# Kernel tuning notes

Measured on AMD Instinct MI355X. Metric: run time of the kernel, lower is better.

## Reference

```python
import jax, jax.numpy as jnp
import numpy as np

B, S, V, E, H, NL, DFF = 16, 16, 64, 64, 8, 4, 2048
L = S * V
DH = E // H
NUM_GRIDS = 100
POI_DIM = 8
OV_DIM = 8


def setup_inputs() -> dict:
    key = jax.random.key(0)
    ks = jax.random.split(key, 32)
    sc = 0.05
    inp = {}
    inp['features'] = jax.random.normal(ks[0], (B, S, V, 3), jnp.float32)
    inp['overlap_tag'] = jax.random.randint(ks[1], (B, S, V), 0, 3)
    inp['poi_id'] = jax.random.randint(ks[2], (B, S, V), 0, NUM_GRIDS + 1)
    # embedders
    inp['W_raw'] = jax.random.normal(ks[3], (3, E), jnp.float32) * sc
    inp['b_raw'] = jnp.zeros((E,), jnp.float32)
    inp['pos_tab'] = jax.random.normal(ks[4], (S, E), jnp.float32) * sc
    inp['type_tab'] = jax.random.normal(ks[5], (V, E), jnp.float32) * sc
    inp['poi_tab'] = jax.random.normal(ks[6], (NUM_GRIDS + 1, POI_DIM), jnp.float32) * sc
    inp['overlap_tab'] = jax.random.normal(ks[7], (3, OV_DIM), jnp.float32) * sc
    inp['W_comb'] = jax.random.normal(ks[8], (E + OV_DIM + POI_DIM, E), jnp.float32) * sc
    inp['b_comb'] = jnp.zeros((E,), jnp.float32)
    # transformer layers (stacked over NL)
    inp['Wqkv'] = jax.random.normal(ks[9], (NL, E, 3 * E), jnp.float32) * sc
    inp['bqkv'] = jnp.zeros((NL, 3 * E), jnp.float32)
    inp['Wo'] = jax.random.normal(ks[10], (NL, E, E), jnp.float32) * sc
    inp['bo'] = jnp.zeros((NL, E), jnp.float32)
    inp['ln1_s'] = jnp.ones((NL, E), jnp.float32)
    inp['ln1_b'] = jnp.zeros((NL, E), jnp.float32)
    inp['W1'] = jax.random.normal(ks[11], (NL, E, DFF), jnp.float32) * sc
    inp['b1'] = jnp.zeros((NL, DFF), jnp.float32)
    inp['W2'] = jax.random.normal(ks[12], (NL, DFF, E), jnp.float32) * sc
    inp['b2'] = jnp.zeros((NL, E), jnp.float32)
    inp['ln2_s'] = jnp.ones((NL, E), jnp.float32)
    inp['ln2_b'] = jnp.zeros((NL, E), jnp.float32)
    inp['W_head'] = jax.random.normal(ks[13], (E, 3), jnp.float32) * sc
    inp['b_head'] = jnp.zeros((3,), jnp.float32)
    return inp


def _layer_norm(x, s, b):
    m = x.mean(-1, keepdims=True)
    v = ((x - m) ** 2).mean(-1, keepdims=True)
    return (x - m) / jnp.sqrt(v + 1e-5) * s + b


def _forward(features, overlap_tag, poi_id, W_raw, b_raw, pos_tab, type_tab,
             poi_tab, overlap_tab, W_comb, b_comb, Wqkv, bqkv, Wo, bo,
             ln1_s, ln1_b, W1, b1, W2, b2, ln2_s, ln2_b, W_head, b_head):
    # padding_idx=0 rows are zero (as in nn.Embedding(padding_idx=0))
    poi_tab = poi_tab.at[0].set(0.0)
    overlap_tab = overlap_tab.at[0].set(0.0)

    zero_mask = (features.sum(-1) == 0).reshape(B, L)  # [B, L]
    ov_idx = jnp.maximum(overlap_tag, 0)
    poi_idx = jnp.maximum(poi_id, 0)

    feat_e = features @ W_raw + b_raw                    # [B,S,V,E]
    concat = jnp.concatenate([feat_e, overlap_tab[ov_idx], poi_tab[poi_idx]], axis=-1)
    x = (concat @ W_comb + b_comb).reshape(B, L, E)      # [B,L,E]

    t_idx = jnp.repeat(jnp.arange(S), V)                 # [L]
    v_idx = jnp.tile(jnp.arange(V), S)                   # [L]
    struct_mask = (t_idx[:, None] != t_idx[None, :]) & (v_idx[:, None] != v_idx[None, :])
    full_mask = struct_mask[None] | zero_mask[:, None, :] | zero_mask[:, :, None]  # [B,L,L]
    bias = jnp.where(full_mask, -jnp.inf, 0.0)[:, None, :, :]  # [B,1,L,L]

    x = x + pos_tab[t_idx][None] + type_tab[v_idx][None]

    scale = 1.0 / jnp.sqrt(jnp.asarray(DH, x.dtype))
    for l in range(NL):
        qkv = x @ Wqkv[l] + bqkv[l]                      # [B,L,3E]
        q, k, v = jnp.split(qkv, 3, axis=-1)
        q = q.reshape(B, L, H, DH)
        k = k.reshape(B, L, H, DH)
        v = v.reshape(B, L, H, DH)
        scores = jnp.einsum('bqhd,bkhd->bhqk', q, k) * scale + bias
        attn = jax.nn.softmax(scores, axis=-1)
        o = jnp.einsum('bhqk,bkhd->bqhd', attn, v).reshape(B, L, E)
        x = _layer_norm(x + o @ Wo[l] + bo[l], ln1_s[l], ln1_b[l])
        ff = jax.nn.relu(x @ W1[l] + b1[l]) @ W2[l] + b2[l]
        x = _layer_norm(x + ff, ln2_s[l], ln2_b[l])

    last = x.reshape(B, S, V, E)[:, -1]                  # [B,V,E]
    return last @ W_head + b_head                        # [B,V,3]


def reference(features, overlap_tag, poi_id, W_raw, b_raw, pos_tab, type_tab,
              poi_tab, overlap_tab, W_comb, b_comb, Wqkv, bqkv, Wo, bo,
              ln1_s, ln1_b, W1, b1, W2, b2, ln2_s, ln2_b, W_head, b_head):
    return _forward(features, overlap_tag, poi_id, W_raw, b_raw, pos_tab, type_tab,
                    poi_tab, overlap_tab, W_comb, b_comb, Wqkv, bqkv, Wo, bo,
                    ln1_s, ln1_b, W1, b1, W2, b2, ln2_s, ln2_b, W_head, b_head)
```

## Files before the change

### kernel.cpp

```cpp
#include <hip/hip_runtime.h>
#include <math.h>

#define BB 16
#define SS 16
#define VVV 64
#define EE 64
#define HHH 8
#define NLAYER 4
#define DFF_ 2048
#define LL 1024
#define BL 16384
#define PERL 131072

typedef __attribute__((ext_vector_type(8))) _Float16 half8;
typedef __attribute__((ext_vector_type(4))) _Float16 half4v;
typedef __attribute__((ext_vector_type(2))) _Float16 half2v;
typedef __attribute__((ext_vector_type(4))) float f32x4;

#if defined(__has_builtin)
#if __has_builtin(__builtin_amdgcn_fdot2)
#define HAVE_FDOT2 1
#endif
#endif

#define SW64(m, k)  (((m) << 6) + ((((k) >> 3) ^ ((m) & 7)) << 3) + ((k) & 7))


__global__ __launch_bounds__(256) void k_prep(
    const float* __restrict__ W1, const float* __restrict__ W2,
    const float* __restrict__ Wqkv, const float* __restrict__ Wo,
    const float* __restrict__ Wcomb,
    _Float16* __restrict__ w1f, _Float16* __restrict__ w2f,
    _Float16* __restrict__ wqkvf, _Float16* __restrict__ wof,
    _Float16* __restrict__ wcombt)
{
  __shared__ float t[64 * 65];
  int bx = blockIdx.x;
  int cc = threadIdx.x & 63, rr = threadIdx.x >> 6;

  if (bx >= 272) {
    int r0 = (bx - 272) * 64;
#pragma unroll
    for (int i = 0; i < 16; i++) {
      int r = i * 4 + rr;
      if (r0 + r < 80) t[r * 65 + cc] = Wcomb[(size_t)(r0 + r) * 64 + cc];
    }
    __syncthreads();
#pragma unroll
    for (int i = 0; i < 16; i++) {
      int c = i * 4 + rr;
      if (r0 + c < 80) wcombt[(size_t)cc * 80 + r0 + c] = (_Float16)t[c * 65 + cc];
    }
    return;
  }

  const float* src; _Float16* dst; int astr;
  if (bx < 128) {
    int l = bx >> 5, g = bx & 31;
    src = W1 + (size_t)l * PERL + g * 64; astr = 2048;
    dst = w1f + (size_t)(l * 32 + g) * 4096;
  } else if (bx < 256) {
    int j = bx - 128; int l = j >> 5, g = j & 31;
    src = W2 + (size_t)l * PERL + (size_t)g * 64 * 64; astr = 64;
    dst = w2f + (size_t)(l * 32 + g) * 4096;
  } else if (bx < 268) {
    int j = bx - 256; int l = j / 3, g = j % 3;
    src = Wqkv + (size_t)l * 64 * 192 + g * 64; astr = 192;
    dst = wqkvf + (size_t)(l * 3 + g) * 4096;
  } else {
    int l = bx - 268;
    src = Wo + (size_t)l * 4096; astr = 64;
    dst = wof + (size_t)l * 4096;
  }
#pragma unroll
  for (int i = 0; i < 16; i++) {
    int a = i * 4 + rr;
    t[cc * 65 + a] = src[(size_t)a * astr + cc];
  }
  __syncthreads();
#pragma unroll
  for (int it = 0; it < 2; it++) {
    int c = threadIdx.x + it * 256;
    int frag = c >> 6, lane = c & 63;
    int m = (frag >> 1) * 16 + (lane & 15);
    int k0 = (frag & 1) * 32 + (lane >> 4) * 8;
    const float* tr = &t[m * 65 + k0];
    half8 h;
#pragma unroll
    for (int j = 0; j < 8; j++) h[j] = (_Float16)tr[j];
    *(half8*)&dst[(size_t)c * 8] = h;
  }
}

__device__ __forceinline__ void qkv_nb(
    const half8 (&af)[2][2], const _Float16* __restrict__ wqkvf,
    const float* __restrict__ bqkv, _Float16* __restrict__ qbuf,
    _Float16* __restrict__ kbuf, _Float16* __restrict__ vbuf,
    int bx, int nb, int wm, int wn, int lane)
{
  int quad = lane >> 4, l15 = lane & 15;
  const _Float16* bt = wqkvf + (size_t)nb * 4096;
  half8 bf[2][2];
#pragma unroll
  for (int nt = 0; nt < 2; nt++)
#pragma unroll
    for (int ks = 0; ks < 2; ks++)
      bf[nt][ks] = *(const half8*)&bt[(size_t)(((wn * 2 + nt) * 2 + ks) * 512) +
                                      lane * 8];
  f32x4 acc[2][2];
#pragma unroll
  for (int mt = 0; mt < 2; mt++)
#pragma unroll
    for (int nt = 0; nt < 2; nt++) {
      float bv = bqkv[nb * 64 + wn * 32 + nt * 16 + l15];
      acc[mt][nt] = (f32x4){bv, bv, bv, bv};
    }
#pragma unroll
  for (int ks = 0; ks < 2; ks++)
#pragma unroll
    for (int mt = 0; mt < 2; mt++)
#pragma unroll
      for (int nt = 0; nt < 2; nt++)
        acc[mt][nt] = __builtin_amdgcn_mfma_f32_16x16x32_f16(
            af[mt][ks], bf[nt][ks], acc[mt][nt], 0, 0, 0);
  _Float16* dst = (nb == 0) ? qbuf : ((nb == 1) ? kbuf : vbuf);
#pragma unroll
  for (int mt = 0; mt < 2; mt++)
#pragma unroll
    for (int nt = 0; nt < 2; nt++) {
      int col = wn * 32 + nt * 16 + l15;
      int h = col >> 3, d = col & 7;
#pragma unroll
      for (int r = 0; r < 4; r++) {
        int row = bx * 64 + wm * 32 + mt * 16 + quad * 4 + r;
        int b = row >> 10, rb = row & 1023;
        dst[((size_t)(b * 8 + h) * 1024 + rb) * 8 + d] = (_Float16)acc[mt][nt][r];
      }
    }
}

__device__ __forceinline__ void ffn_load(
    const _Float16* __restrict__ w1f, const _Float16* __restrict__ w2f, int g,
    half8 (&a1)[2][2], half8 (&b2w)[2][2], int wm, int wn, int lane)
{
  const _Float16* w1t_ = w1f + (size_t)g * 4096;
  const _Float16* w2t_ = w2f + (size_t)g * 4096;
#pragma unroll
  for (int ht = 0; ht < 2; ht++)
#pragma unroll
    for (int ks = 0; ks < 2; ks++)
      a1[ht][ks] = *(const half8*)&w1t_[(size_t)(((wm * 2 + ht) * 2 + ks) * 512) +
                                        lane * 8];
#pragma unroll
  for (int nt = 0; nt < 2; nt++)
#pragma unroll
    for (int ks = 0; ks < 2; ks++)
      b2w[nt][ks] = *(const half8*)&w2t_[(size_t)(((wn * 2 + nt) * 2 + ks) * 512) +
                                         lane * 8];
}

__device__ __forceinline__ void ffn_step(
    const half8 (&a1)[2][2], const half8 (&b2w)[2][2], const half8 (&xb)[2][2],
    _Float16* hsbuf, const float* __restrict__ b1, int g, f32x4 (&acc)[2][2],
    int wm, int wn, int lane)
{
  int quad = lane >> 4, l15 = lane & 15;
  f32x4 hacc[2][2];
#pragma unroll
  for (int ht = 0; ht < 2; ht++)
#pragma unroll
    for (int mt = 0; mt < 2; mt++) hacc[ht][mt] = (f32x4){0.f, 0.f, 0.f, 0.f};
#pragma unroll
  for (int ks = 0; ks < 2; ks++)
#pragma unroll
    for (int ht = 0; ht < 2; ht++)
#pragma unroll
      for (int mt = 0; mt < 2; mt++)
        hacc[ht][mt] = __builtin_amdgcn_mfma_f32_16x16x32_f16(
            a1[ht][ks], xb[mt][ks], hacc[ht][mt], 0, 0, 0);
#pragma unroll
  for (int ht = 0; ht < 2; ht++) {
    float4 bb = *(const float4*)&b1[g * 64 + wm * 32 + ht * 16 + quad * 4];
#pragma unroll
    for (int mt = 0; mt < 2; mt++) {
      f32x4 hv = hacc[ht][mt];
      half4v hp = (half4v){
          (_Float16)fmaxf(hv[0] + bb.x, 0.f), (_Float16)fmaxf(hv[1] + bb.y, 0.f),
          (_Float16)fmaxf(hv[2] + bb.z, 0.f), (_Float16)fmaxf(hv[3] + bb.w, 0.f)};
      *(half4v*)&hsbuf[SW64(wn * 32 + mt * 16 + l15,
                            wm * 32 + ht * 16 + quad * 4)] = hp;
    }
  }
  __syncthreads();
#pragma unroll
  for (int ks = 0; ks < 2; ks++)
#pragma unroll
    for (int mt = 0; mt < 2; mt++) {
      half8 a2 = *(const half8*)&hsbuf[SW64(wm * 32 + mt * 16 + l15,
                                            ks * 32 + quad * 8)];
#pragma unroll
      for (int nt = 0; nt < 2; nt++)
        acc[mt][nt] = __builtin_amdgcn_mfma_f32_16x16x32_f16(a2, b2w[nt][ks],
                                                             acc[mt][nt], 0, 0, 0);
    }
}

__global__ __launch_bounds__(256) void k_embqkv(
    const float* __restrict__ features, const int* __restrict__ ovtag,
    const int* __restrict__ poiid, const float* __restrict__ W_raw,
    const float* __restrict__ b_raw, const float* __restrict__ ov_tab,
    const float* __restrict__ poi_tab, const _Float16* __restrict__ wcombt,
    const float* __restrict__ b_comb, const float* __restrict__ pos_tab,
    const float* __restrict__ type_tab, float* __restrict__ x1,
    float* __restrict__ zm, const _Float16* __restrict__ wqkvf,
    const float* __restrict__ bqkv, _Float16* __restrict__ qbuf,
    _Float16* __restrict__ kbuf, _Float16* __restrict__ vbuf)
{
  constexpr int KP = 104;
  __shared__ _Float16 As[64 * KP];
  __shared__ _Float16 Bs[64 * KP];
  __shared__ _Float16 xs[4096];
  int tid = threadIdx.x;
  int bx = blockIdx.x;
  int m0 = bx * 64;
  int wave = tid >> 6, lane = tid & 63, quad = lane >> 4, l15 = lane & 15;
  int wm = wave >> 1, wn = wave & 1;
  for (int p = tid; p < 1536; p += 256) {
    int r = p / 24, s = p - r * 24; int c = s * 4;
    int row = m0 + r;
    float f0 = features[row * 3 + 0];
    float f1 = features[row * 3 + 1];
    float f2 = features[row * 3 + 2];
    if (s == 0) zm[row] = ((f0 + f1 + f2) == 0.f) ? 1.f : 0.f;
    half4v h;
#pragma unroll
    for (int j = 0; j < 4; j++) {
      int cc = c + j; float v;
      if (cc < 64) {
        v = b_raw[cc] + f0 * W_raw[cc] + f1 * W_raw[64 + cc] + f2 * W_raw[128 + cc];
      } else if (cc < 72) {
        int tt = ovtag[row]; v = (tt <= 0) ? 0.f : ov_tab[tt * 8 + cc - 64];
      } else if (cc < 80) {
        int tt = poiid[row]; v = (tt <= 0) ? 0.f : poi_tab[tt * 8 + cc - 72];
      } else v = 0.f;
      h[j] = (_Float16)v;
    }
    *(half4v*)&As[r * KP + c] = h;
  }
  for (int p = tid; p < 1536; p += 256) {
    int r = p / 24, s = p - r * 24; int c = s * 4;
    half4v h = (half4v){0, 0, 0, 0};
    if (c < 80) h = *(const half4v*)&wcombt[r * 80 + c];
    *(half4v*)&Bs[r * KP + c] = h;
  }
  __syncthreads();
  f32x4 acc[2][2];
#pragma unroll
  for (int mt = 0; mt < 2; mt++)
#pragma unroll
    for (int nt = 0; nt < 2; nt++) {
      float bv = b_comb[wn * 32 + nt * 16 + l15];
      acc[mt][nt] = (f32x4){bv, bv, bv, bv};
    }
#pragma unroll
  for (int ks = 0; ks < 3; ks++) {
    half8 af[2], bf[2];
#pragma unroll
    for (int mt = 0; mt < 2; mt++)
      af[mt] = *(const half8*)&As[(wm * 32 + mt * 16 + l15) * KP + ks * 32 + quad * 8];
#pragma unroll
    for (int nt = 0; nt < 2; nt++)
      bf[nt] = *(const half8*)&Bs[(wn * 32 + nt * 16 + l15) * KP + ks * 32 + quad * 8];
#pragma unroll
    for (int mt = 0; mt < 2; mt++)
#pragma unroll
      for (int nt = 0; nt < 2; nt++)
        acc[mt][nt] = __builtin_amdgcn_mfma_f32_16x16x32_f16(af[mt], bf[nt],
                                                             acc[mt][nt], 0, 0, 0);
  }
#pragma unroll
  for (int mt = 0; mt < 2; mt++)
#pragma unroll
    for (int nt = 0; nt < 2; nt++)
#pragma unroll
      for (int r = 0; r < 4; r++) {
        int lrow = wm * 32 + mt * 16 + quad * 4 + r;
        int row = m0 + lrow;
        int col = wn * 32 + nt * 16 + l15;
        int l = row & (LL - 1);
        float v = acc[mt][nt][r] +
            pos_tab[(l >> 6) * 64 + col] + type_tab[(l & 63) * 64 + col];
        x1[(size_t)row * 64 + col] = v;
        xs[SW64(lrow, col)] = (_Float16)v;
      }
  __syncthreads();
  half8 af[2][2];
#pragma unroll
  for (int mt = 0; mt < 2; mt++)
#pragma unroll
    for (int ks = 0; ks < 2; ks++)
      af[mt][ks] = *(const half8*)&xs[SW64(wm * 32 + mt * 16 + l15,
                                           ks * 32 + quad * 8)];
  for (int nb = 0; nb < 3; nb++)
    qkv_nb(af, wqkvf, bqkv, qbuf, kbuf, vbuf, bx, nb, wm, wn, lane);
}

__global__ __launch_bounds__(256) void k_attn2(
    const _Float16* __restrict__ qbuf, const _Float16* __restrict__ kbuf,
    const _Float16* __restrict__ vbuf, const float* __restrict__ zm,
    _Float16* __restrict__ obuf)
{
  __shared__ _Float16 Ks[1024 * 8];
  __shared__ _Float16 Vs[1024 * 8];
  __shared__ float zs[1024];
  int blk = blockIdx.x;
  int qb = blk & 3, h = (blk >> 2) & 7, b = blk >> 5;
  int qrow = qb * 256 + threadIdx.x;
  half8 qh = *(const half8*)&qbuf[(size_t)(b * 8 + h) * 8192 + (size_t)qrow * 8];
  const _Float16* kb = kbuf + (size_t)(b * 8 + h) * 8192;
  const _Float16* vb = vbuf + (size_t)(b * 8 + h) * 8192;
  for (int p = threadIdx.x; p < 1024; p += 256) {
    *(half8*)&Ks[p * 8] = *(const half8*)&kb[p * 8];
    *(half8*)&Vs[p * 8] = *(const half8*)&vb[p * 8];
    zs[p] = zm[b * LL + p];
  }
  __syncthreads();
  int tq = qrow >> 6, vq = qrow & 63;
  const float scale = 0.3535533905932738f;
  float m = -INFINITY, lsum = 0.f;
  float acc[8] = {0.f, 0.f, 0.f, 0.f, 0.f, 0.f, 0.f, 0.f};
  bool zmq = (zs[qrow] != 0.f);

  auto attend = [&](int k) {
    if (zs[k] != 0.f) return;
    half8 kk = *(const half8*)&Ks[k * 8];
    float s = 0.f;
#ifdef HAVE_FDOT2
#pragma unroll
    for (int j = 0; j < 4; j++) {
      half2v qa = (half2v){qh[2 * j], qh[2 * j + 1]};
      half2v ka = (half2v){kk[2 * j], kk[2 * j + 1]};
      s = __builtin_amdgcn_fdot2(qa, ka, s, false);
    }
#else
#pragma unroll
    for (int j = 0; j < 8; j++) s += (float)qh[j] * (float)kk[j];
#endif
    s *= scale;
    half8 vv = *(const half8*)&Vs[k * 8];
    if (s <= m) {
      float p = __expf(s - m);
      lsum += p;
#pragma unroll
      for (int d = 0; d < 8; d++) acc[d] += p * (float)vv[d];
    } else {
      float r = __expf(m - s);
      lsum = lsum * r + 1.f;
#pragma unroll
      for (int d = 0; d < 8; d++) acc[d] = acc[d] * r + (float)vv[d];
      m = s;
    }
  };

  if (!zmq) {
    for (int vv = 0; vv < 64; vv++) attend(tq * 64 + vv);
    for (int tt = 0; tt < 16; tt++) {
      if (tt == tq) continue;
      attend(tt * 64 + vq);
    }
  }
  float inv = 1.f / lsum;
  half8 o;
#pragma unroll
  for (int d = 0; d < 8; d++) o[d] = (_Float16)(acc[d] * inv);
  size_t tile = (size_t)(b * 16 + (qrow >> 6));
  int frag = ((qrow >> 4) & 3) * 2 + (h >> 2);
  int flane = (h & 3) * 16 + (qrow & 15);
  *(half8*)&obuf[tile * 4096 + frag * 512 + flane * 8] = o;
}

__global__ __launch_bounds__(512) void k_layer(
    const _Float16* __restrict__ obuf, const _Float16* __restrict__ wof,
    const float* __restrict__ bo, float* __restrict__ x1,
    const float* __restrict__ ln1_s, const float* __restrict__ ln1_b,
    const _Float16* __restrict__ w1f, const _Float16* __restrict__ w2f,
    const float* __restrict__ b1, const float* __restrict__ b2,
    const float* __restrict__ ln2_s, const float* __restrict__ ln2_b,
    const _Float16* __restrict__ wqkvf, const float* __restrict__ bqkv,
    _Float16* __restrict__ qbuf, _Float16* __restrict__ kbuf,
    _Float16* __restrict__ vbuf, int doqkv,
    const float* __restrict__ Wh, const float* __restrict__ bh,
    float* __restrict__ out)
{
  __shared__ float ots[64 * 68];
  __shared__ _Float16 xs[4096];
  __shared__ float x2f[4096];
  __shared__ _Float16 hs[2][2][4096];
  int tid = threadIdx.x;
  int bx = blockIdx.x;
  int wave = tid >> 6, lane = tid & 63;
  int quad = lane >> 4, l15 = lane & 15;
  int grp = wave >> 2, w4 = wave & 3;
  int wm = w4 >> 1, wn = w4 & 1;

  {
    const _Float16* ot = obuf + (size_t)bx * 4096;
    int mq = grp * 2 + wm;
    half8 af[2], bf[2][2];
#pragma unroll
    for (int ks = 0; ks < 2; ks++)
      af[ks] = *(const half8*)&ot[(size_t)((mq * 2 + ks) * 512) + lane * 8];
#pragma unroll
    for (int nt = 0; nt < 2; nt++)
#pragma unroll
      for (int ks = 0; ks < 2; ks++)
        bf[nt][ks] = *(const half8*)&wof[(size_t)(((wn * 2 + nt) * 2 + ks) * 512) +
                                         lane * 8];
    f32x4 acc[2];
#pragma unroll
    for (int nt = 0; nt < 2; nt++) {
      float bv = bo[wn * 32 + nt * 16 + l15];
      acc[nt] = (f32x4){bv, bv, bv, bv};
    }
#pragma unroll
    for (int ks = 0; ks < 2; ks++)
#pragma unroll
      for (int nt = 0; nt < 2; nt++)
        acc[nt] = __builtin_amdgcn_mfma_f32_16x16x32_f16(af[ks], bf[nt][ks],
                                                         acc[nt], 0, 0, 0);
#pragma unroll
    for (int nt = 0; nt < 2; nt++)
#pragma unroll
      for (int r = 0; r < 4; r++)
        ots[(mq * 16 + quad * 4 + r) * 68 + wn * 32 + nt * 16 + l15] = acc[nt][r];
  }
  __syncthreads();
  for (int i = 0; i < 8; i++) {
    int row = wave * 8 + i;
    size_t off = (size_t)(bx * 64 + row) * 64 + lane;
    float val = ots[row * 68 + lane] + x1[off];
    float sum = val;
#pragma unroll
    for (int o = 32; o > 0; o >>= 1) sum += __shfl_xor(sum, o);
    float mean = sum * (1.f / 64.f);
    float d = val - mean;
    float sq = d * d;
#pragma unroll
    for (int o = 32; o > 0; o >>= 1) sq += __shfl_xor(sq, o);
    float xv = d * rsqrtf(sq * (1.f / 64.f) + 1e-5f) * ln1_s[lane] + ln1_b[lane];
    x2f[row * 64 + lane] = xv;
    xs[SW64(row, lane)] = (_Float16)xv;
  }
  __syncthreads();

  half8 xb[2][2];
#pragma unroll
  for (int mt = 0; mt < 2; mt++)
#pragma unroll
    for (int ks = 0; ks < 2; ks++)
      xb[mt][ks] = *(const half8*)&xs[SW64(wn * 32 + mt * 16 + l15,
                                           ks * 32 + quad * 8)];
  f32x4 acc[2][2];
#pragma unroll
  for (int mt = 0; mt < 2; mt++)
#pragma unroll
    for (int nt = 0; nt < 2; nt++) {
      float bv = (grp == 0) ? b2[wn * 32 + nt * 16 + l15] : 0.f;
      acc[mt][nt] = (f32x4){bv, bv, bv, bv};
    }
  half8 a1x[2][2], b2x[2][2], a1y[2][2], b2y[2][2];
  ffn_load(w1f, w2f, grp, a1x, b2x, wm, wn, lane);
  for (int ii = 0; ii < 8; ii++) {
    ffn_load(w1f, w2f, ii * 4 + 2 + grp, a1y, b2y, wm, wn, lane);
    ffn_step(a1x, b2x, xb, &hs[grp][0][0], b1, ii * 4 + grp, acc, wm, wn, lane);
    if (ii < 7) ffn_load(w1f, w2f, ii * 4 + 4 + grp, a1x, b2x, wm, wn, lane);
    ffn_step(a1y, b2y, xb, &hs[grp][1][0], b1, ii * 4 + 2 + grp, acc, wm, wn, lane);
  }
  __syncthreads();
  if (grp == 0) {
#pragma unroll
    for (int mt = 0; mt < 2; mt++)
#pragma unroll
      for (int nt = 0; nt < 2; nt++)
#pragma unroll
        for (int r = 0; r < 4; r++)
          ots[(wm * 32 + mt * 16 + quad * 4 + r) * 68 + wn * 32 + nt * 16 + l15] =
              acc[mt][nt][r];
  }
  __syncthreads();
  if (grp == 1) {
#pragma unroll
    for (int mt = 0; mt < 2; mt++)
#pragma unroll
      for (int nt = 0; nt < 2; nt++)
#pragma unroll
        for (int r = 0; r < 4; r++)
          ots[(wm * 32 + mt * 16 + quad * 4 + r) * 68 + wn * 32 + nt * 16 + l15] +=
              acc[mt][nt][r];
  }
  __syncthreads();
  for (int i = 0; i < 8; i++) {
    int row = wave * 8 + i;
    size_t off = (size_t)(bx * 64 + row) * 64 + lane;
    float val = ots[row * 68 + lane] + x2f[row * 64 + lane];
    float sum = val;
#pragma unroll
    for (int o = 32; o > 0; o >>= 1) sum += __shfl_xor(sum, o);
    float mean = sum * (1.f / 64.f);
    float d = val - mean;
    float sq = d * d;
#pragma unroll
    for (int o = 32; o > 0; o >>= 1) sq += __shfl_xor(sq, o);
    float xv = d * rsqrtf(sq * (1.f / 64.f) + 1e-5f) * ln2_s[lane] + ln2_b[lane];
    x1[off] = xv;
    x2f[row * 64 + lane] = xv;
    xs[SW64(row, lane)] = (_Float16)xv;
  }
  if (!doqkv) {
    __syncthreads();
    if ((bx & 15) == 15 && tid < 192) {
      int b = bx >> 4;
      int v = tid / 3, j = tid - v * 3;
      float a = bh[j];
      for (int e = 0; e < 64; e++)
        a += x2f[v * 64 + e] * Wh[e * 3 + j];
      out[((size_t)(b * 64 + v)) * 3 + j] = a;
    }
    return;
  }
  __syncthreads();
  half8 af[2][2];
#pragma unroll
  for (int mt = 0; mt < 2; mt++)
#pragma unroll
    for (int ks = 0; ks < 2; ks++)
      af[mt][ks] = *(const half8*)&xs[SW64(wm * 32 + mt * 16 + l15,
                                           ks * 32 + quad * 8)];
  for (int nb = grp; nb < 3; nb += 2)
    qkv_nb(af, wqkvf, bqkv, qbuf, kbuf, vbuf, bx, nb, wm, wn, lane);
}

extern "C" void kernel_launch(void* const* d_in, const int* in_sizes, int n_in,
                              void* d_out, int out_size, void* d_ws, size_t ws_size,
                              hipStream_t stream) {
  const float* features = (const float*)d_in[0];
  const int*   ovtag    = (const int*)d_in[1];
  const int*   poiid    = (const int*)d_in[2];
  const float* W_raw    = (const float*)d_in[3];
  const float* b_raw    = (const float*)d_in[4];
  const float* pos_tab  = (const float*)d_in[5];
  const float* type_tab = (const float*)d_in[6];
  const float* poi_tab  = (const float*)d_in[7];
  const float* ov_tab   = (const float*)d_in[8];
  const float* W_comb   = (const float*)d_in[9];
  const float* b_comb   = (const float*)d_in[10];
  const float* Wqkv     = (const float*)d_in[11];
  const float* bqkv     = (const float*)d_in[12];
  const float* Wo       = (const float*)d_in[13];
  const float* bo       = (const float*)d_in[14];
  const float* ln1_s    = (const float*)d_in[15];
  const float* ln1_b    = (const float*)d_in[16];
  const float* W1       = (const float*)d_in[17];
  const float* b1       = (const float*)d_in[18];
  const float* W2       = (const float*)d_in[19];
  const float* b2       = (const float*)d_in[20];
  const float* ln2_s    = (const float*)d_in[21];
  const float* ln2_b    = (const float*)d_in[22];
  const float* W_head   = (const float*)d_in[23];
  const float* b_head   = (const float*)d_in[24];
  float* out = (float*)d_out;
  float* ws  = (float*)d_ws;

  float* zm  = ws;
  float* x1  = zm + BL;
  _Float16* qbuf   = (_Float16*)(x1 + (size_t)BL * 64);
  _Float16* kbuf   = qbuf + (size_t)BL * 64;
  _Float16* vbuf   = kbuf + (size_t)BL * 64;
  _Float16* obuf16 = vbuf + (size_t)BL * 64;
  _Float16* wcombt = obuf16 + (size_t)BL * 64;
  _Float16* w1f    = wcombt + 5120;
  _Float16* w2f    = w1f + (size_t)NLAYER * PERL;
  _Float16* wqkvf  = w2f + (size_t)NLAYER * PERL;
  _Float16* wof    = wqkvf + (size_t)NLAYER * 3 * 4096;

  k_prep<<<274, 256, 0, stream>>>(W1, W2, Wqkv, Wo, W_comb,
                                  w1f, w2f, wqkvf, wof, wcombt);
  k_embqkv<<<256, 256, 0, stream>>>(features, ovtag, poiid, W_raw, b_raw,
                                    ov_tab, poi_tab, wcombt, b_comb,
                                    pos_tab, type_tab, x1, zm,
                                    wqkvf, bqkv, qbuf, kbuf, vbuf);
  for (int l = 0; l < NLAYER; l++) {
    k_attn2<<<512, 256, 0, stream>>>(qbuf, kbuf, vbuf, zm, obuf16);
    int doqkv = (l < NLAYER - 1);
    k_layer<<<256, 512, 0, stream>>>(
        obuf16, wof + (size_t)l * 4096, bo + l * EE, x1,
        ln1_s + l * EE, ln1_b + l * EE,
        w1f + (size_t)l * PERL, w2f + (size_t)l * PERL,
        b1 + l * DFF_, b2 + l * EE,
        ln2_s + l * EE, ln2_b + l * EE,
        wqkvf + (size_t)(l + 1 < NLAYER ? l + 1 : 0) * 3 * 4096,
        bqkv + (l + 1 < NLAYER ? l + 1 : 0) * 192,
        qbuf, kbuf, vbuf, doqkv, W_head, b_head, out);
  }
}
```

Measured before the change: 317.4 us.

## Halve per-block row tiles in layer and attention kernels to double grid size

The fused layer kernel now handles 32 rows per block with 256 threads instead of 64 rows with 512, and asks for two blocks per CU. Its FFN, output projection and QKV projection are re-indexed to match, with the QKV projection inlined per wave. The attention kernel uses 128-thread blocks over 1024 blocks, and its online softmax update becomes a branchless max/rescale form. The aim is more blocks for better CU occupancy and less divergence, at the cost of loading each K/V head twice as often and reading FFN weights once per 32 rows rather than per 64.

Result: faster. 309.0 us (-2.7%).

```diff
diff --git a/kernel.cpp b/kernel.cpp
--- a/kernel.cpp
+++ b/kernel.cpp
@@ -139,9 +139,9 @@
     }
 }
 
-__device__ __forceinline__ void ffn_load(
+__device__ __forceinline__ void ffn_load2(
     const _Float16* __restrict__ w1f, const _Float16* __restrict__ w2f, int g,
-    half8 (&a1)[2][2], half8 (&b2w)[2][2], int wm, int wn, int lane)
+    half8 (&a1)[2][2], half8 (&b2w)[2][2], int wn, int lane)
 {
   const _Float16* w1t_ = w1f + (size_t)g * 4096;
   const _Float16* w2t_ = w2f + (size_t)g * 4096;
@@ -149,7 +149,7 @@
   for (int ht = 0; ht < 2; ht++)
 #pragma unroll
     for (int ks = 0; ks < 2; ks++)
-      a1[ht][ks] = *(const half8*)&w1t_[(size_t)(((wm * 2 + ht) * 2 + ks) * 512) +
+      a1[ht][ks] = *(const half8*)&w1t_[(size_t)(((wn * 2 + ht) * 2 + ks) * 512) +
                                         lane * 8];
 #pragma unroll
   for (int nt = 0; nt < 2; nt++)
@@ -159,10 +159,10 @@
                                          lane * 8];
 }
 
-__device__ __forceinline__ void ffn_step(
+__device__ __forceinline__ void ffn_step2(
     const half8 (&a1)[2][2], const half8 (&b2w)[2][2], const half8 (&xb)[2][2],
     _Float16* hsbuf, const float* __restrict__ b1, int g, f32x4 (&acc)[2][2],
-    int wm, int wn, int lane)
+    int wn, int lane)
 {
   int quad = lane >> 4, l15 = lane & 15;
   f32x4 hacc[2][2];
@@ -180,15 +180,14 @@
             a1[ht][ks], xb[mt][ks], hacc[ht][mt], 0, 0, 0);
 #pragma unroll
   for (int ht = 0; ht < 2; ht++) {
-    float4 bb = *(const float4*)&b1[g * 64 + wm * 32 + ht * 16 + quad * 4];
+    float4 bb = *(const float4*)&b1[g * 64 + wn * 32 + ht * 16 + quad * 4];
 #pragma unroll
     for (int mt = 0; mt < 2; mt++) {
       f32x4 hv = hacc[ht][mt];
       half4v hp = (half4v){
           (_Float16)fmaxf(hv[0] + bb.x, 0.f), (_Float16)fmaxf(hv[1] + bb.y, 0.f),
           (_Float16)fmaxf(hv[2] + bb.z, 0.f), (_Float16)fmaxf(hv[3] + bb.w, 0.f)};
-      *(half4v*)&hsbuf[SW64(wn * 32 + mt * 16 + l15,
-                            wm * 32 + ht * 16 + quad * 4)] = hp;
+      *(half4v*)&hsbuf[SW64(mt * 16 + l15, wn * 32 + ht * 16 + quad * 4)] = hp;
     }
   }
   __syncthreads();
@@ -196,8 +195,7 @@
   for (int ks = 0; ks < 2; ks++)
 #pragma unroll
     for (int mt = 0; mt < 2; mt++) {
-      half8 a2 = *(const half8*)&hsbuf[SW64(wm * 32 + mt * 16 + l15,
-                                            ks * 32 + quad * 8)];
+      half8 a2 = *(const half8*)&hsbuf[SW64(mt * 16 + l15, ks * 32 + quad * 8)];
 #pragma unroll
       for (int nt = 0; nt < 2; nt++)
         acc[mt][nt] = __builtin_amdgcn_mfma_f32_16x16x32_f16(a2, b2w[nt][ks],
@@ -305,7 +303,7 @@
     qkv_nb(af, wqkvf, bqkv, qbuf, kbuf, vbuf, bx, nb, wm, wn, lane);
 }
 
-__global__ __launch_bounds__(256) void k_attn2(
+__global__ __launch_bounds__(128) void k_attn3(
     const _Float16* __restrict__ qbuf, const _Float16* __restrict__ kbuf,
     const _Float16* __restrict__ vbuf, const float* __restrict__ zm,
     _Float16* __restrict__ obuf)
@@ -314,12 +312,12 @@
   __shared__ _Float16 Vs[1024 * 8];
   __shared__ float zs[1024];
   int blk = blockIdx.x;
-  int qb = blk & 3, h = (blk >> 2) & 7, b = blk >> 5;
-  int qrow = qb * 256 + threadIdx.x;
+  int qb = blk & 7, h = (blk >> 3) & 7, b = blk >> 6;
+  int qrow = qb * 128 + threadIdx.x;
   half8 qh = *(const half8*)&qbuf[(size_t)(b * 8 + h) * 8192 + (size_t)qrow * 8];
   const _Float16* kb = kbuf + (size_t)(b * 8 + h) * 8192;
   const _Float16* vb = vbuf + (size_t)(b * 8 + h) * 8192;
-  for (int p = threadIdx.x; p < 1024; p += 256) {
+  for (int p = threadIdx.x; p < 1024; p += 128) {
     *(half8*)&Ks[p * 8] = *(const half8*)&kb[p * 8];
     *(half8*)&Vs[p * 8] = *(const half8*)&vb[p * 8];
     zs[p] = zm[b * LL + p];
@@ -348,18 +346,13 @@
 #endif
     s *= scale;
     half8 vv = *(const half8*)&Vs[k * 8];
-    if (s <= m) {
-      float p = __expf(s - m);
-      lsum += p;
-#pragma unroll
-      for (int d = 0; d < 8; d++) acc[d] += p * (float)vv[d];
-    } else {
-      float r = __expf(m - s);
-      lsum = lsum * r + 1.f;
-#pragma unroll
-      for (int d = 0; d < 8; d++) acc[d] = acc[d] * r + (float)vv[d];
-      m = s;
-    }
+    float nm = fmaxf(m, s);
+    float r = __expf(m - nm);
+    float p = __expf(s - nm);
+    lsum = lsum * r + p;
+#pragma unroll
+    for (int d = 0; d < 8; d++) acc[d] = acc[d] * r + p * (float)vv[d];
+    m = nm;
   };
 
   if (!zmq) {
@@ -379,7 +372,7 @@
   *(half8*)&obuf[tile * 4096 + frag * 512 + flane * 8] = o;
 }
 
-__global__ __launch_bounds__(512) void k_layer(
+__global__ __launch_bounds__(256, 2) void k_layer2(
     const _Float16* __restrict__ obuf, const _Float16* __restrict__ wof,
     const float* __restrict__ bo, float* __restrict__ x1,
     const float* __restrict__ ln1_s, const float* __restrict__ ln1_b,
@@ -392,24 +385,24 @@
     const float* __restrict__ Wh, const float* __restrict__ bh,
     float* __restrict__ out)
 {
-  __shared__ float ots[64 * 68];
-  __shared__ _Float16 xs[4096];
-  __shared__ float x2f[4096];
-  __shared__ _Float16 hs[2][2][4096];
+  __shared__ float ots[32 * 68];
+  __shared__ _Float16 xs[2048];
+  __shared__ float x2f[2048];
+  __shared__ _Float16 hs[2][2][2048];
   int tid = threadIdx.x;
   int bx = blockIdx.x;
+  int r0 = bx * 32;
   int wave = tid >> 6, lane = tid & 63;
   int quad = lane >> 4, l15 = lane & 15;
-  int grp = wave >> 2, w4 = wave & 3;
-  int wm = w4 >> 1, wn = w4 & 1;
+  int grp = wave >> 1, wn = wave & 1;
 
   {
-    const _Float16* ot = obuf + (size_t)bx * 4096;
-    int mq = grp * 2 + wm;
+    const _Float16* ot = obuf + (size_t)(bx >> 1) * 4096;
+    int mt_g = (bx & 1) * 2 + grp;
     half8 af[2], bf[2][2];
 #pragma unroll
     for (int ks = 0; ks < 2; ks++)
-      af[ks] = *(const half8*)&ot[(size_t)((mq * 2 + ks) * 512) + lane * 8];
+      af[ks] = *(const half8*)&ot[(size_t)((mt_g * 2 + ks) * 512) + lane * 8];
 #pragma unroll
     for (int nt = 0; nt < 2; nt++)
 #pragma unroll
@@ -432,12 +425,12 @@
     for (int nt = 0; nt < 2; nt++)
 #pragma unroll
       for (int r = 0; r < 4; r++)
-        ots[(mq * 16 + quad * 4 + r) * 68 + wn * 32 + nt * 16 + l15] = acc[nt][r];
+        ots[(grp * 16 + quad * 4 + r) * 68 + wn * 32 + nt * 16 + l15] = acc[nt][r];
   }
   __syncthreads();
   for (int i = 0; i < 8; i++) {
     int row = wave * 8 + i;
-    size_t off = (size_t)(bx * 64 + row) * 64 + lane;
+    size_t off = (size_t)(r0 + row) * 64 + lane;
     float val = ots[row * 68 + lane] + x1[off];
     float sum = val;
 #pragma unroll
@@ -458,8 +451,7 @@
   for (int mt = 0; mt < 2; mt++)
 #pragma unroll
     for (int ks = 0; ks < 2; ks++)
-      xb[mt][ks] = *(const half8*)&xs[SW64(wn * 32 + mt * 16 + l15,
-                                           ks * 32 + quad * 8)];
+      xb[mt][ks] = *(const half8*)&xs[SW64(mt * 16 + l15, ks * 32 + quad * 8)];
   f32x4 acc[2][2];
 #pragma unroll
   for (int mt = 0; mt < 2; mt++)
@@ -469,12 +461,12 @@
       acc[mt][nt] = (f32x4){bv, bv, bv, bv};
     }
   half8 a1x[2][2], b2x[2][2], a1y[2][2], b2y[2][2];
-  ffn_load(w1f, w2f, grp, a1x, b2x, wm, wn, lane);
+  ffn_load2(w1f, w2f, grp, a1x, b2x, wn, lane);
   for (int ii = 0; ii < 8; ii++) {
-    ffn_load(w1f, w2f, ii * 4 + 2 + grp, a1y, b2y, wm, wn, lane);
-    ffn_step(a1x, b2x, xb, &hs[grp][0][0], b1, ii * 4 + grp, acc, wm, wn, lane);
-    if (ii < 7) ffn_load(w1f, w2f, ii * 4 + 4 + grp, a1x, b2x, wm, wn, lane);
-    ffn_step(a1y, b2y, xb, &hs[grp][1][0], b1, ii * 4 + 2 + grp, acc, wm, wn, lane);
+    ffn_load2(w1f, w2f, ii * 4 + 2 + grp, a1y, b2y, wn, lane);
+    ffn_step2(a1x, b2x, xb, &hs[grp][0][0], b1, ii * 4 + grp, acc, wn, lane);
+    if (ii < 7) ffn_load2(w1f, w2f, ii * 4 + 4 + grp, a1x, b2x, wn, lane);
+    ffn_step2(a1y, b2y, xb, &hs[grp][1][0], b1, ii * 4 + 2 + grp, acc, wn, lane);
   }
   __syncthreads();
   if (grp == 0) {
@@ -484,7 +476,7 @@
       for (int nt = 0; nt < 2; nt++)
 #pragma unroll
         for (int r = 0; r < 4; r++)
-          ots[(wm * 32 + mt * 16 + quad * 4 + r) * 68 + wn * 32 + nt * 16 + l15] =
+          ots[(mt * 16 + quad * 4 + r) * 68 + wn * 32 + nt * 16 + l15] =
               acc[mt][nt][r];
   }
   __syncthreads();
@@ -495,13 +487,13 @@
       for (int nt = 0; nt < 2; nt++)
 #pragma unroll
         for (int r = 0; r < 4; r++)
-          ots[(wm * 32 + mt * 16 + quad * 4 + r) * 68 + wn * 32 + nt * 16 + l15] +=
+          ots[(mt * 16 + quad * 4 + r) * 68 + wn * 32 + nt * 16 + l15] +=
               acc[mt][nt][r];
   }
   __syncthreads();
   for (int i = 0; i < 8; i++) {
     int row = wave * 8 + i;
-    size_t off = (size_t)(bx * 64 + row) * 64 + lane;
+    size_t off = (size_t)(r0 + row) * 64 + lane;
     float val = ots[row * 68 + lane] + x2f[row * 64 + lane];
     float sum = val;
 #pragma unroll
@@ -518,13 +510,14 @@
   }
   if (!doqkv) {
     __syncthreads();
-    if ((bx & 15) == 15 && tid < 192) {
-      int b = bx >> 4;
-      int v = tid / 3, j = tid - v * 3;
+    if ((bx & 31) >= 30 && tid < 96) {
+      int b = bx >> 5;
+      int i = tid / 3, j = tid - i * 3;
+      int vglob = (bx & 1) * 32 + i;
       float a = bh[j];
       for (int e = 0; e < 64; e++)
-        a += x2f[v * 64 + e] * Wh[e * 3 + j];
-      out[((size_t)(b * 64 + v)) * 3 + j] = a;
+        a += x2f[i * 64 + e] * Wh[e * 3 + j];
+      out[((size_t)(b * 64 + vglob)) * 3 + j] = a;
     }
     return;
   }
@@ -534,10 +527,37 @@
   for (int mt = 0; mt < 2; mt++)
 #pragma unroll
     for (int ks = 0; ks < 2; ks++)
-      af[mt][ks] = *(const half8*)&xs[SW64(wm * 32 + mt * 16 + l15,
-                                           ks * 32 + quad * 8)];
-  for (int nb = grp; nb < 3; nb += 2)
-    qkv_nb(af, wqkvf, bqkv, qbuf, kbuf, vbuf, bx, nb, wm, wn, lane);
+      af[mt][ks] = *(const half8*)&xs[SW64(mt * 16 + l15, ks * 32 + quad * 8)];
+  for (int nb = 0; nb < 3; nb++) {
+    const _Float16* bt = wqkvf + (size_t)nb * 4096;
+    half8 bf[2];
+#pragma unroll
+    for (int ks = 0; ks < 2; ks++)
+      bf[ks] = *(const half8*)&bt[(size_t)((wave * 2 + ks) * 512) + lane * 8];
+    f32x4 qacc[2];
+#pragma unroll
+    for (int mt = 0; mt < 2; mt++) {
+      float bv = bqkv[nb * 64 + wave * 16 + l15];
+      qacc[mt] = (f32x4){bv, bv, bv, bv};
+    }
+#pragma unroll
+    for (int ks = 0; ks < 2; ks++)
+#pragma unroll
+      for (int mt = 0; mt < 2; mt++)
+        qacc[mt] = __builtin_amdgcn_mfma_f32_16x16x32_f16(af[mt][ks], bf[ks],
+                                                          qacc[mt], 0, 0, 0);
+    _Float16* dst = (nb == 0) ? qbuf : ((nb == 1) ? kbuf : vbuf);
+    int col = wave * 16 + l15;
+    int h = col >> 3, d = col & 7;
+#pragma unroll
+    for (int mt = 0; mt < 2; mt++)
+#pragma unroll
+      for (int r = 0; r < 4; r++) {
+        int row = r0 + mt * 16 + quad * 4 + r;
+        int b = row >> 10, rb = row & 1023;
+        dst[((size_t)(b * 8 + h) * 1024 + rb) * 8 + d] = (_Float16)qacc[mt][r];
+      }
+  }
 }
 
 extern "C" void kernel_launch(void* const* d_in, const int* in_sizes, int n_in,
@@ -590,9 +610,9 @@
                                     pos_tab, type_tab, x1, zm,
                                     wqkvf, bqkv, qbuf, kbuf, vbuf);
   for (int l = 0; l < NLAYER; l++) {
-    k_attn2<<<512, 256, 0, stream>>>(qbuf, kbuf, vbuf, zm, obuf16);
+    k_attn3<<<1024, 128, 0, stream>>>(qbuf, kbuf, vbuf, zm, obuf16);
     int doqkv = (l < NLAYER - 1);
-    k_layer<<<256, 512, 0, stream>>>(
+    k_layer2<<<512, 256, 0, stream>>>(
         obuf16, wof + (size_t)l * 4096, bo + l * EE, x1,
         ln1_s + l * EE, ln1_b + l * EE,
         w1f + (size_t)l * PERL, w2f + (size_t)l * PERL,
```
